# Kernel tuning notes

Hardware: AMD Instinct MI355X
Metric: run time of the kernel (lower is better)

The kernel has to match this reference:

```python
import jax, jax.numpy as jnp
import numpy as np

HEADS = 8
KEY_DIM = 32
EPS = 1e-5


def layernorm(x, gamma, beta, eps=EPS):
    mu = jnp.mean(x, axis=-1, keepdims=True)
    var = jnp.mean(jnp.square(x - mu), axis=-1, keepdims=True)
    return (x - mu) * jax.lax.rsqrt(var + eps) * gamma + beta


def setup_inputs() -> dict:
    key = jax.random.key(0)
    ks = jax.random.split(key, 6)
    B, H, W, C = 16, 32, 32, 256
    inner = HEADS * KEY_DIM  # 256
    s = 1.0 / np.sqrt(C)
    return {
        "x": jax.random.normal(ks[0], (B, H, W, C), jnp.float32),
        "gamma": jnp.ones((C,), jnp.float32),
        "beta": jnp.zeros((C,), jnp.float32),
        "Wq": jax.random.normal(ks[1], (C, inner), jnp.float32) * s,
        "bq": jnp.zeros((inner,), jnp.float32),
        "Wk": jax.random.normal(ks[2], (C, inner), jnp.float32) * s,
        "bk": jnp.zeros((inner,), jnp.float32),
        "Wv": jax.random.normal(ks[3], (C, inner), jnp.float32) * s,
        "bv": jnp.zeros((inner,), jnp.float32),
        "Wp": jax.random.normal(ks[4], (inner, C), jnp.float32) * s,
        "bp": jnp.zeros((C,), jnp.float32),
    }


def reference(x, gamma, beta, Wq, bq, Wk, bk, Wv, bv, Wp, bp):
    B, H, W, C = x.shape
    N = H * W
    h, d = HEADS, KEY_DIM
    X = layernorm(x, gamma, beta)              # [B,H,W,C]
    Xf = X.reshape(B, N, C)                    # 1x1 conv == per-token linear
    Q = (Xf @ Wq + bq).reshape(B, N, h, d)
    K = (Xf @ Wk + bk).reshape(B, N, h, d)
    V = (Xf @ Wv + bv).reshape(B, N, h, d)
    scale = jnp.asarray(d, x.dtype) ** -0.5
    scores = jnp.einsum('bnhd,bmhd->bhnm', Q, K) * scale
    A = jax.nn.softmax(scores, axis=-1)        # [B,h,N,N]
    Y = jnp.einsum('bhnm,bmhd->bnhd', A, V).reshape(B, N, h * d)
    out = (Y @ Wp + bp).reshape(B, H, W, C)
    return out
```

## Files before the change

### kernel.cpp

```cpp
#include <hip/hip_runtime.h>
#include <hip/hip_bf16.h>

typedef __bf16 bf16_t;
typedef __attribute__((ext_vector_type(8))) __bf16 bf16x8;
typedef __attribute__((ext_vector_type(4))) float f32x4;
typedef __attribute__((ext_vector_type(4))) short s16x4;

#define GLDS16(g, l) __builtin_amdgcn_global_load_lds( \
    (const __attribute__((address_space(1))) unsigned int*)(g), \
    (__attribute__((address_space(3))) unsigned int*)(l), 16, 0, 0)

__device__ __forceinline__ float fexp2(float x) {
#if __has_builtin(__builtin_amdgcn_exp2f)
  return __builtin_amdgcn_exp2f(x);
#else
  return exp2f(x);
#endif
}

#define QSCALE (0.17677669529663688f * 1.4426950408889634f)

__global__ __launch_bounds__(256) void wtr_kernel(
    const float* __restrict__ Wq, const float* __restrict__ Wk,
    const float* __restrict__ Wv, const float* __restrict__ Wp,
    bf16_t* __restrict__ Wt)
{
  const int idx = blockIdx.x * 256 + threadIdx.x;
  const int mat = idx >> 16;
  const int e   = idx & 65535;
  const int k   = e >> 8;
  const int n   = e & 255;
  const float* W = (mat == 0) ? Wq : (mat == 1) ? Wk : (mat == 2) ? Wv : Wp;
  Wt[(size_t)mat * 65536 + n * 256 + k] = (bf16_t)W[e];
}

__global__ __launch_bounds__(256) void ln_kernel(
    const float* __restrict__ x, const float* __restrict__ gamma,
    const float* __restrict__ beta, bf16_t* __restrict__ Xln)
{
  const int wave = threadIdx.x >> 6, lane = threadIdx.x & 63;
  const int tok = blockIdx.x * 4 + wave;
  const float4 v = *reinterpret_cast<const float4*>(x + (size_t)tok * 256 + lane * 4);
  float s1 = v.x + v.y + v.z + v.w;
  float s2 = v.x*v.x + v.y*v.y + v.z*v.z + v.w*v.w;
  #pragma unroll
  for (int off = 1; off < 64; off <<= 1) {
    s1 += __shfl_xor(s1, off);
    s2 += __shfl_xor(s2, off);
  }
  const float mean = s1 * (1.0f/256.0f);
  const float var  = s2 * (1.0f/256.0f) - mean*mean;
  const float rstd = rsqrtf(var + 1e-5f);
  const float4 g  = *reinterpret_cast<const float4*>(gamma + lane*4);
  const float4 be = *reinterpret_cast<const float4*>(beta  + lane*4);
  union { bf16_t h4[4]; unsigned long long u; } pk;
  pk.h4[0] = (bf16_t)((v.x-mean)*rstd*g.x + be.x);
  pk.h4[1] = (bf16_t)((v.y-mean)*rstd*g.y + be.y);
  pk.h4[2] = (bf16_t)((v.z-mean)*rstd*g.z + be.z);
  pk.h4[3] = (bf16_t)((v.w-mean)*rstd*g.w + be.w);
  *reinterpret_cast<unsigned long long*>(Xln + (size_t)tok*256 + lane*4) = pk.u;
}

template<int MODE>
__global__ __launch_bounds__(256) void gemm_kernel(
    const bf16_t* __restrict__ A, const bf16_t* __restrict__ Wt,
    const float* __restrict__ b0, const float* __restrict__ b1,
    const float* __restrict__ b2,
    bf16_t* __restrict__ Qb, bf16_t* __restrict__ Kb, bf16_t* __restrict__ Vt,
    float* __restrict__ Fout)
{
  __shared__ __align__(16) bf16_t As[128*64];
  __shared__ __align__(16) bf16_t Bs[128*64];
  const int tid  = threadIdx.x;
  const int lane = tid & 63, wave = tid >> 6;
  const int lg = lane >> 4, li = lane & 15;
  const int wm = wave >> 1, wn = wave & 1;
  const int mt = blockIdx.x;
  const int nt = blockIdx.y;
  int mat, nbase;
  const bf16_t* Bm;
  if (MODE == 0) { mat = nt >> 1; nbase = (nt & 1) * 128; Bm = Wt + (size_t)mat * 65536; }
  else           { mat = 3;       nbase = nt * 128;       Bm = Wt; }

  f32x4 acc[4][4] = {};

  for (int kt = 0; kt < 4; ++kt) {
    __syncthreads();
    #pragma unroll
    for (int i = 0; i < 4; ++i) {
      const int idx = i*256 + tid;
      const int row = idx >> 3, ck = idx & 7;
      const int cs = ck ^ (row & 7);
      GLDS16(A + (size_t)(mt*128 + row)*256 + kt*64 + cs*8, As + idx*8);
    }
    #pragma unroll
    for (int i = 0; i < 4; ++i) {
      const int idx = i*256 + tid;
      const int row = idx >> 3, ck = idx & 7;
      const int cs = ck ^ (row & 7);
      GLDS16(Bm + (size_t)(nbase + row)*256 + kt*64 + cs*8, Bs + idx*8);
    }
    __syncthreads();
    #pragma unroll
    for (int kk = 0; kk < 2; ++kk) {
      bf16x8 af[4], bfv[4];
      #pragma unroll
      for (int mi = 0; mi < 4; ++mi) {
        const int row = wm*64 + mi*16 + li;
        const int c = (kk*4 + lg) ^ (row & 7);
        af[mi] = *reinterpret_cast<const bf16x8*>(As + row*64 + c*8);
      }
      #pragma unroll
      for (int ni = 0; ni < 4; ++ni) {
        const int row = wn*64 + ni*16 + li;
        const int c = (kk*4 + lg) ^ (row & 7);
        bfv[ni] = *reinterpret_cast<const bf16x8*>(Bs + row*64 + c*8);
      }
      #pragma unroll
      for (int mi = 0; mi < 4; ++mi)
        #pragma unroll
        for (int ni = 0; ni < 4; ++ni)
          acc[mi][ni] = __builtin_amdgcn_mfma_f32_16x16x32_bf16(af[mi], bfv[ni], acc[mi][ni], 0, 0, 0);
    }
  }

  if (MODE == 0) {
    const float* bias = (mat == 0) ? b0 : (mat == 1) ? b1 : b2;
    if (mat < 2) {
      bf16_t* Out = (mat == 0) ? Qb : Kb;
      const float osc = (mat == 0) ? QSCALE : 1.0f;
      #pragma unroll
      for (int mi = 0; mi < 4; ++mi)
        #pragma unroll
        for (int ni = 0; ni < 4; ++ni) {
          const int col = nbase + wn*64 + ni*16 + li;
          const float bb = bias[col];
          #pragma unroll
          for (int r = 0; r < 4; ++r) {
            const int row = mt*128 + wm*64 + mi*16 + lg*4 + r;
            Out[(size_t)row*256 + col] = (bf16_t)((acc[mi][ni][r] + bb) * osc);
          }
        }
    } else {
      #pragma unroll
      for (int mi = 0; mi < 4; ++mi)
        #pragma unroll
        for (int ni = 0; ni < 4; ++ni) {
          const int col = nbase + wn*64 + ni*16 + li;
          const int hh = col >> 5, dd = col & 31;
          const float bb = bias[col];
          const int row0 = mt*128 + wm*64 + mi*16 + lg*4;
          const int bi = row0 >> 10, nn = row0 & 1023;
          union { bf16_t h4[4]; unsigned long long u; } pk;
          #pragma unroll
          for (int r = 0; r < 4; ++r) pk.h4[r] = (bf16_t)(acc[mi][ni][r] + bb);
          *reinterpret_cast<unsigned long long*>(
              Vt + ((size_t)(bi*8 + hh)*32 + dd)*1024 + nn) = pk.u;
        }
    }
  } else {
    #pragma unroll
    for (int mi = 0; mi < 4; ++mi)
      #pragma unroll
      for (int ni = 0; ni < 4; ++ni) {
        const int col = nbase + wn*64 + ni*16 + li;
        const float bb = b0[col];
        #pragma unroll
        for (int r = 0; r < 4; ++r) {
          const int row = mt*128 + wm*64 + mi*16 + lg*4 + r;
          Fout[(size_t)row*256 + col] = acc[mi][ni][r] + bb;
        }
      }
  }
}

__global__ __launch_bounds__(256, 6) void attn_kernel(
    const bf16_t* __restrict__ Qb, const bf16_t* __restrict__ Kb,
    const bf16_t* __restrict__ Vt, bf16_t* __restrict__ Yb)
{
  __shared__ __align__(16) char Ks[2][4096];
  __shared__ __align__(16) char Vs[2][4096];
  const int tid  = threadIdx.x;
  const int wave = tid >> 6, lane = tid & 63;
  const int lg = lane >> 4, li = lane & 15;
  const int gid = blockIdx.x;
  const int qt = (gid >> 3) & 15;
  const int bh = ((gid >> 7) << 3) | (gid & 7);
  const int b  = bh >> 3, hh = bh & 7;
  const int tok0 = b*1024 + qt*64 + wave*16;

  const bf16x8 qf = *reinterpret_cast<const bf16x8*>(
      Qb + (size_t)(tok0 + li)*256 + hh*32 + lg*8);

  const int kt_ = tid >> 2, ks_ = tid & 3;
  const bf16_t* Ksrc = Kb + (size_t)(b*1024 + kt_)*256 + hh*32
                          + ((ks_ ^ ((kt_ >> 1) & 3)) * 8);
  const int vd_ = tid >> 3, vs_ = tid & 7;
  const bf16_t* Vsrc = Vt + ((size_t)bh*32 + vd_)*1024
                          + ((vs_ ^ (vd_ & 7)) * 8);

  const int kof = li*64 + ((lg ^ ((li >> 1) & 3)) * 16);
  int vof[4];
  #pragma unroll
  for (int ct = 0; ct < 4; ++ct)
    vof[ct] = li*128 + (((ct*2 + (lg >> 1)) ^ (li & 7)) * 16) + (lg & 1)*8;

  const f32x4 fz = {0.f, 0.f, 0.f, 0.f};
  f32x4 acc0 = fz, acc1 = fz;
  float m = 0.f;
  float lrow = 0.f;

  GLDS16(Ksrc, &Ks[0][tid*16]);
  GLDS16(Vsrc, &Vs[0][tid*16]);
  __syncthreads();

  #pragma unroll 2
  for (int mc = 0; mc < 16; ++mc) {
    const int cur = mc & 1;
    if (mc < 15) {
      GLDS16(Ksrc + (size_t)(mc+1)*16384, &Ks[cur^1][tid*16]);
      GLDS16(Vsrc + (mc+1)*64,            &Vs[cur^1][tid*16]);
    }
    const char* kb = &Ks[cur][0];
    const char* vb = &Vs[cur][0];
    f32x4 s[4];
    #pragma unroll
    for (int ct = 0; ct < 4; ++ct) {
      const bf16x8 kfrag = *reinterpret_cast<const bf16x8*>(kb + kof + ct*1024);
      s[ct] = __builtin_amdgcn_mfma_f32_16x16x32_bf16(kfrag, qf, fz, 0, 0, 0);
    }
    s16x4 vq0[4], vq1[4];
    #pragma unroll
    for (int ct = 0; ct < 4; ++ct) {
      vq0[ct] = *reinterpret_cast<const s16x4*>(vb + vof[ct]);
      vq1[ct] = *reinterpret_cast<const s16x4*>(vb + vof[ct] + 16*128);
    }
    float mx0 = fmaxf(fmaxf(s[0][0], s[0][1]), fmaxf(s[0][2], s[0][3]));
    float mx1 = fmaxf(fmaxf(s[1][0], s[1][1]), fmaxf(s[1][2], s[1][3]));
    float mx2 = fmaxf(fmaxf(s[2][0], s[2][1]), fmaxf(s[2][2], s[2][3]));
    float mx3 = fmaxf(fmaxf(s[3][0], s[3][1]), fmaxf(s[3][2], s[3][3]));
    const float pmax = fmaxf(fmaxf(mx0, mx1), fmaxf(mx2, mx3));
    if (!__all(pmax - m <= 8.0f)) {
      float rmx = pmax;
      rmx = fmaxf(rmx, __shfl_xor(rmx, 16));
      rmx = fmaxf(rmx, __shfl_xor(rmx, 32));
      const float mnew = fmaxf(m, rmx);
      const float sf = fexp2(m - mnew);
      lrow *= sf;
      #pragma unroll
      for (int r = 0; r < 4; ++r) { acc0[r] *= sf; acc1[r] *= sf; }
      m = mnew;
    }
    float psum = 0.f;
    #pragma unroll
    for (int ct = 0; ct < 4; ++ct) {
      #pragma unroll
      for (int r = 0; r < 4; ++r)
        s[ct][r] = fexp2(s[ct][r] - m);
      psum += (s[ct][0] + s[ct][1]) + (s[ct][2] + s[ct][3]);
    }
    lrow += psum;
    #pragma unroll
    for (int ct = 0; ct < 4; ++ct) {
      union { bf16_t h4[4]; s16x4 v; } pk;
      #pragma unroll
      for (int r = 0; r < 4; ++r) pk.h4[r] = (bf16_t)s[ct][r];
      acc0 = __builtin_amdgcn_mfma_f32_16x16x16bf16_1k(vq0[ct], pk.v, acc0, 0, 0, 0);
      acc1 = __builtin_amdgcn_mfma_f32_16x16x16bf16_1k(vq1[ct], pk.v, acc1, 0, 0, 0);
    }
    __syncthreads();
  }

  float lsum = lrow;
  lsum += __shfl_xor(lsum, 16);
  lsum += __shfl_xor(lsum, 32);
  const float inv = 1.0f / lsum;
  union { bf16_t h4[4]; unsigned long long u; } o0, o1;
  #pragma unroll
  for (int r = 0; r < 4; ++r) {
    o0.h4[r] = (bf16_t)(acc0[r]*inv);
    o1.h4[r] = (bf16_t)(acc1[r]*inv);
  }
  bf16_t* yp = Yb + (size_t)(tok0 + li)*256 + hh*32;
  *reinterpret_cast<unsigned long long*>(yp + lg*4)      = o0.u;
  *reinterpret_cast<unsigned long long*>(yp + 16 + lg*4) = o1.u;
}

extern "C" void kernel_launch(void* const* d_in, const int* in_sizes, int n_in,
                              void* d_out, int out_size, void* d_ws, size_t ws_size,
                              hipStream_t stream) {
  const float* x     = (const float*)d_in[0];
  const float* gamma = (const float*)d_in[1];
  const float* beta  = (const float*)d_in[2];
  const float* Wq    = (const float*)d_in[3];
  const float* bq    = (const float*)d_in[4];
  const float* Wk    = (const float*)d_in[5];
  const float* bk    = (const float*)d_in[6];
  const float* Wv    = (const float*)d_in[7];
  const float* bv    = (const float*)d_in[8];
  const float* Wp    = (const float*)d_in[9];
  const float* bp    = (const float*)d_in[10];
  float* out = (float*)d_out;

  char* ws = (char*)d_ws;
  bf16_t* Wt  = (bf16_t*)(ws);
  bf16_t* Xln = (bf16_t*)(ws + 524288);
  bf16_t* Qb  = (bf16_t*)(ws + 8912896);
  bf16_t* Kb  = (bf16_t*)(ws + 17301504);
  bf16_t* Vt  = (bf16_t*)(ws + 25690112);
  bf16_t* Yb  = Xln;

  wtr_kernel<<<1024, 256, 0, stream>>>(Wq, Wk, Wv, Wp, Wt);
  ln_kernel<<<4096, 256, 0, stream>>>(x, gamma, beta, Xln);
  gemm_kernel<0><<<dim3(128, 6), 256, 0, stream>>>(
      Xln, Wt, bq, bk, bv, Qb, Kb, Vt, nullptr);
  attn_kernel<<<2048, 256, 0, stream>>>(Qb, Kb, Vt, Yb);
  gemm_kernel<1><<<dim3(128, 2), 256, 0, stream>>>(
      Yb, Wt + 3*65536, bp, nullptr, nullptr, nullptr, nullptr, nullptr, out);
}
```

Measured before the change: 81.11 us.

## Process two 16-row query tiles per wave in attention to reuse K/V fragments

Each wave in the attention kernel now handles 32 query rows instead of 16, keeping two independent online-softmax states and four accumulators. The same K and V fragments read from LDS feed both query tiles, so the global-to-LDS K/V traffic per query is halved and the grid drops from 2048 to 1024 blocks. The cost is higher register pressure: the occupancy hint falls from 6 to 4 blocks per CU, and there are fewer blocks to spread across the CUs.

After: 79.42 us. 2.1% less time.

```diff
diff --git a/kernel.cpp b/kernel.cpp
--- a/kernel.cpp
+++ b/kernel.cpp
@@ -174,7 +174,7 @@
   }
 }
 
-__global__ __launch_bounds__(256, 6) void attn_kernel(
+__global__ __launch_bounds__(256, 4) void attn_kernel(
     const bf16_t* __restrict__ Qb, const bf16_t* __restrict__ Kb,
     const bf16_t* __restrict__ Vt, bf16_t* __restrict__ Yb)
 {
@@ -184,13 +184,15 @@
   const int wave = tid >> 6, lane = tid & 63;
   const int lg = lane >> 4, li = lane & 15;
   const int gid = blockIdx.x;
-  const int qt = (gid >> 3) & 15;
-  const int bh = ((gid >> 7) << 3) | (gid & 7);
+  const int qt = (gid >> 3) & 7;
+  const int bh = ((gid >> 6) << 3) | (gid & 7);
   const int b  = bh >> 3, hh = bh & 7;
-  const int tok0 = b*1024 + qt*64 + wave*16;
-
-  const bf16x8 qf = *reinterpret_cast<const bf16x8*>(
+  const int tok0 = b*1024 + qt*128 + wave*32;
+
+  const bf16x8 qf0 = *reinterpret_cast<const bf16x8*>(
       Qb + (size_t)(tok0 + li)*256 + hh*32 + lg*8);
+  const bf16x8 qf1 = *reinterpret_cast<const bf16x8*>(
+      Qb + (size_t)(tok0 + 16 + li)*256 + hh*32 + lg*8);
 
   const int kt_ = tid >> 2, ks_ = tid & 3;
   const bf16_t* Ksrc = Kb + (size_t)(b*1024 + kt_)*256 + hh*32
@@ -206,9 +208,10 @@
     vof[ct] = li*128 + (((ct*2 + (lg >> 1)) ^ (li & 7)) * 16) + (lg & 1)*8;
 
   const f32x4 fz = {0.f, 0.f, 0.f, 0.f};
-  f32x4 acc0 = fz, acc1 = fz;
-  float m = 0.f;
-  float lrow = 0.f;
+  f32x4 acc00 = fz, acc01 = fz;
+  f32x4 acc10 = fz, acc11 = fz;
+  float m0 = 0.f, m1 = 0.f;
+  float lrow0 = 0.f, lrow1 = 0.f;
 
   GLDS16(Ksrc, &Ks[0][tid*16]);
   GLDS16(Vsrc, &Vs[0][tid*16]);
@@ -223,11 +226,12 @@
     }
     const char* kb = &Ks[cur][0];
     const char* vb = &Vs[cur][0];
-    f32x4 s[4];
+    f32x4 s0[4], s1[4];
     #pragma unroll
     for (int ct = 0; ct < 4; ++ct) {
       const bf16x8 kfrag = *reinterpret_cast<const bf16x8*>(kb + kof + ct*1024);
-      s[ct] = __builtin_amdgcn_mfma_f32_16x16x32_bf16(kfrag, qf, fz, 0, 0, 0);
+      s0[ct] = __builtin_amdgcn_mfma_f32_16x16x32_bf16(kfrag, qf0, fz, 0, 0, 0);
+      s1[ct] = __builtin_amdgcn_mfma_f32_16x16x32_bf16(kfrag, qf1, fz, 0, 0, 0);
     }
     s16x4 vq0[4], vq1[4];
     #pragma unroll
@@ -235,55 +239,92 @@
       vq0[ct] = *reinterpret_cast<const s16x4*>(vb + vof[ct]);
       vq1[ct] = *reinterpret_cast<const s16x4*>(vb + vof[ct] + 16*128);
     }
-    float mx0 = fmaxf(fmaxf(s[0][0], s[0][1]), fmaxf(s[0][2], s[0][3]));
-    float mx1 = fmaxf(fmaxf(s[1][0], s[1][1]), fmaxf(s[1][2], s[1][3]));
-    float mx2 = fmaxf(fmaxf(s[2][0], s[2][1]), fmaxf(s[2][2], s[2][3]));
-    float mx3 = fmaxf(fmaxf(s[3][0], s[3][1]), fmaxf(s[3][2], s[3][3]));
-    const float pmax = fmaxf(fmaxf(mx0, mx1), fmaxf(mx2, mx3));
-    if (!__all(pmax - m <= 8.0f)) {
-      float rmx = pmax;
-      rmx = fmaxf(rmx, __shfl_xor(rmx, 16));
-      rmx = fmaxf(rmx, __shfl_xor(rmx, 32));
-      const float mnew = fmaxf(m, rmx);
-      const float sf = fexp2(m - mnew);
-      lrow *= sf;
-      #pragma unroll
-      for (int r = 0; r < 4; ++r) { acc0[r] *= sf; acc1[r] *= sf; }
-      m = mnew;
-    }
-    float psum = 0.f;
+    {
+      float mxa = fmaxf(fmaxf(s0[0][0], s0[0][1]), fmaxf(s0[0][2], s0[0][3]));
+      float mxb = fmaxf(fmaxf(s0[1][0], s0[1][1]), fmaxf(s0[1][2], s0[1][3]));
+      float mxc = fmaxf(fmaxf(s0[2][0], s0[2][1]), fmaxf(s0[2][2], s0[2][3]));
+      float mxd = fmaxf(fmaxf(s0[3][0], s0[3][1]), fmaxf(s0[3][2], s0[3][3]));
+      const float pmax = fmaxf(fmaxf(mxa, mxb), fmaxf(mxc, mxd));
+      if (!__all(pmax - m0 <= 8.0f)) {
+        float rmx = pmax;
+        rmx = fmaxf(rmx, __shfl_xor(rmx, 16));
+        rmx = fmaxf(rmx, __shfl_xor(rmx, 32));
+        const float mnew = fmaxf(m0, rmx);
+        const float sf = fexp2(m0 - mnew);
+        lrow0 *= sf;
+        #pragma unroll
+        for (int r = 0; r < 4; ++r) { acc00[r] *= sf; acc01[r] *= sf; }
+        m0 = mnew;
+      }
+      float psum = 0.f;
+      #pragma unroll
+      for (int ct = 0; ct < 4; ++ct) {
+        #pragma unroll
+        for (int r = 0; r < 4; ++r)
+          s0[ct][r] = fexp2(s0[ct][r] - m0);
+        psum += (s0[ct][0] + s0[ct][1]) + (s0[ct][2] + s0[ct][3]);
+      }
+      lrow0 += psum;
+    }
+    {
+      float mxa = fmaxf(fmaxf(s1[0][0], s1[0][1]), fmaxf(s1[0][2], s1[0][3]));
+      float mxb = fmaxf(fmaxf(s1[1][0], s1[1][1]), fmaxf(s1[1][2], s1[1][3]));
+      float mxc = fmaxf(fmaxf(s1[2][0], s1[2][1]), fmaxf(s1[2][2], s1[2][3]));
+      float mxd = fmaxf(fmaxf(s1[3][0], s1[3][1]), fmaxf(s1[3][2], s1[3][3]));
+      const float pmax = fmaxf(fmaxf(mxa, mxb), fmaxf(mxc, mxd));
+      if (!__all(pmax - m1 <= 8.0f)) {
+        float rmx = pmax;
+        rmx = fmaxf(rmx, __shfl_xor(rmx, 16));
+        rmx = fmaxf(rmx, __shfl_xor(rmx, 32));
+        const float mnew = fmaxf(m1, rmx);
+        const float sf = fexp2(m1 - mnew);
+        lrow1 *= sf;
+        #pragma unroll
+        for (int r = 0; r < 4; ++r) { acc10[r] *= sf; acc11[r] *= sf; }
+        m1 = mnew;
+      }
+      float psum = 0.f;
+      #pragma unroll
+      for (int ct = 0; ct < 4; ++ct) {
+        #pragma unroll
+        for (int r = 0; r < 4; ++r)
+          s1[ct][r] = fexp2(s1[ct][r] - m1);
+        psum += (s1[ct][0] + s1[ct][1]) + (s1[ct][2] + s1[ct][3]);
+      }
+      lrow1 += psum;
+    }
     #pragma unroll
     for (int ct = 0; ct < 4; ++ct) {
-      #pragma unroll
-      for (int r = 0; r < 4; ++r)
-        s[ct][r] = fexp2(s[ct][r] - m);
-      psum += (s[ct][0] + s[ct][1]) + (s[ct][2] + s[ct][3]);
-    }
-    lrow += psum;
-    #pragma unroll
-    for (int ct = 0; ct < 4; ++ct) {
-      union { bf16_t h4[4]; s16x4 v; } pk;
-      #pragma unroll
-      for (int r = 0; r < 4; ++r) pk.h4[r] = (bf16_t)s[ct][r];
-      acc0 = __builtin_amdgcn_mfma_f32_16x16x16bf16_1k(vq0[ct], pk.v, acc0, 0, 0, 0);
-      acc1 = __builtin_amdgcn_mfma_f32_16x16x16bf16_1k(vq1[ct], pk.v, acc1, 0, 0, 0);
+      union { bf16_t h4[4]; s16x4 v; } p0, p1;
+      #pragma unroll
+      for (int r = 0; r < 4; ++r) { p0.h4[r] = (bf16_t)s0[ct][r];
+                                    p1.h4[r] = (bf16_t)s1[ct][r]; }
+      acc00 = __builtin_amdgcn_mfma_f32_16x16x16bf16_1k(vq0[ct], p0.v, acc00, 0, 0, 0);
+      acc01 = __builtin_amdgcn_mfma_f32_16x16x16bf16_1k(vq1[ct], p0.v, acc01, 0, 0, 0);
+      acc10 = __builtin_amdgcn_mfma_f32_16x16x16bf16_1k(vq0[ct], p1.v, acc10, 0, 0, 0);
+      acc11 = __builtin_amdgcn_mfma_f32_16x16x16bf16_1k(vq1[ct], p1.v, acc11, 0, 0, 0);
     }
     __syncthreads();
   }
 
-  float lsum = lrow;
-  lsum += __shfl_xor(lsum, 16);
-  lsum += __shfl_xor(lsum, 32);
-  const float inv = 1.0f / lsum;
-  union { bf16_t h4[4]; unsigned long long u; } o0, o1;
+  float ls0 = lrow0, ls1 = lrow1;
+  ls0 += __shfl_xor(ls0, 16); ls0 += __shfl_xor(ls0, 32);
+  ls1 += __shfl_xor(ls1, 16); ls1 += __shfl_xor(ls1, 32);
+  const float inv0 = 1.0f / ls0, inv1 = 1.0f / ls1;
+  union { bf16_t h4[4]; unsigned long long u; } o00, o01, o10, o11;
   #pragma unroll
   for (int r = 0; r < 4; ++r) {
-    o0.h4[r] = (bf16_t)(acc0[r]*inv);
-    o1.h4[r] = (bf16_t)(acc1[r]*inv);
-  }
-  bf16_t* yp = Yb + (size_t)(tok0 + li)*256 + hh*32;
-  *reinterpret_cast<unsigned long long*>(yp + lg*4)      = o0.u;
-  *reinterpret_cast<unsigned long long*>(yp + 16 + lg*4) = o1.u;
+    o00.h4[r] = (bf16_t)(acc00[r]*inv0);
+    o01.h4[r] = (bf16_t)(acc01[r]*inv0);
+    o10.h4[r] = (bf16_t)(acc10[r]*inv1);
+    o11.h4[r] = (bf16_t)(acc11[r]*inv1);
+  }
+  bf16_t* yp0 = Yb + (size_t)(tok0 + li)*256 + hh*32;
+  bf16_t* yp1 = Yb + (size_t)(tok0 + 16 + li)*256 + hh*32;
+  *reinterpret_cast<unsigned long long*>(yp0 + lg*4)      = o00.u;
+  *reinterpret_cast<unsigned long long*>(yp0 + 16 + lg*4) = o01.u;
+  *reinterpret_cast<unsigned long long*>(yp1 + lg*4)      = o10.u;
+  *reinterpret_cast<unsigned long long*>(yp1 + 16 + lg*4) = o11.u;
 }
 
 extern "C" void kernel_launch(void* const* d_in, const int* in_sizes, int n_in,
@@ -314,7 +355,7 @@
   ln_kernel<<<4096, 256, 0, stream>>>(x, gamma, beta, Xln);
   gemm_kernel<0><<<dim3(128, 6), 256, 0, stream>>>(
       Xln, Wt, bq, bk, bv, Qb, Kb, Vt, nullptr);
-  attn_kernel<<<2048, 256, 0, stream>>>(Qb, Kb, Vt, Yb);
+  attn_kernel<<<1024, 256, 0, stream>>>(Qb, Kb, Vt, Yb);
   gemm_kernel<1><<<dim3(128, 2), 256, 0, stream>>>(
       Yb, Wt + 3*65536, bp, nullptr, nullptr, nullptr, nullptr, nullptr, out);
 }
```
